# Kernel tuning notes

Measured on AMD Instinct MI355X. Metric: run time of the kernel, lower is better.

## Reference

```python
import jax, jax.numpy as jnp
import numpy as np
import math

DIM = 128
B, S = 4, 4096


def setup_inputs() -> dict:
    key = jax.random.key(0)
    k1, k2, k3, k4 = jax.random.split(key, 4)
    inp = jax.random.normal(k1, (B, S, DIM), dtype=jnp.float32)
    w_k = jax.random.normal(k2, (DIM, DIM), dtype=jnp.float32) / math.sqrt(DIM)
    w_v = jax.random.normal(k3, (DIM, DIM), dtype=jnp.float32) / math.sqrt(DIM)
    mask = jax.random.randint(k4, (B, S, S), 0, 2).astype(jnp.bool_)
    return {"inp": inp, "w_k": w_k, "w_v": w_v, "mask": mask}


def reference(inp, w_k, w_v, mask):
    # key/val projections: BottleLinear(dim, dim, bias=False) -> x @ W^T
    key = jnp.einsum('bsd,ed->bse', inp, w_k)   # [B,S,D]
    val = jnp.einsum('bsd,ed->bse', inp, w_v)   # [B,S,D]
    # score = inp @ key^T / sqrt(dim)           # [B,S,S]
    score = jnp.einsum('bqd,bkd->bqk', inp, key) / math.sqrt(inp.shape[-1])
    score = jnp.where(mask, -jnp.inf, score)
    attn = jax.nn.softmax(score, axis=2)        # [B,S,S]
    out = jnp.einsum('bqk,bkd->bqd', attn, val) # [B,S,D]
    return (out, attn)
```

## Files before the change

### kernel.cpp

```cpp
#include <hip/hip_runtime.h>
#include <hip/hip_fp16.h>
#include <math.h>

#define DIM 128
#define SQL 4096
#define NBATCH 4
#define NROW (NBATCH*SQL)
#define SCALE 0.08838834764831845f
#define KSPLIT 4
#define PROJBLK (NROW/16)
#define MASKBLK 8192

typedef _Float16 f16;
typedef _Float16 f16x4 __attribute__((ext_vector_type(4)));
typedef _Float16 f16x8 __attribute__((ext_vector_type(8)));
typedef float f32x4 __attribute__((ext_vector_type(4)));

__device__ __forceinline__ f32x4 mfma16(f16x8 a, f16x8 b, f32x4 c) {
  return __builtin_amdgcn_mfma_f32_16x16x32_f16(a, b, c, 0, 0, 0);
}

__global__ __launch_bounds__(256) void prep(const float* __restrict__ inp,
                                            const float* __restrict__ wk,
                                            const float* __restrict__ wv,
                                            const void* __restrict__ mask,
                                            f16* __restrict__ q16,
                                            f16* __restrict__ kfrag,
                                            f16* __restrict__ vfrag,
                                            unsigned long long* __restrict__ mbits,
                                            int n) {
  __shared__ float s_in[16][DIM];
  __shared__ __align__(16) f16 s_vt[DIM][16];
  __shared__ __align__(16) f16 s_kf[2048];
  __shared__ int s_is32;
  const int t = threadIdx.x;

  if (blockIdx.x < PROJBLK) {
    const int rowbase = blockIdx.x * 16;
    const int e = t & 127;
    const int half_ = t >> 7;

    for (int r = half_; r < 16; r += 2)
      s_in[r][e] = inp[(size_t)(rowbase + r) * DIM + e];
    __syncthreads();

    float ak[8], av[8];
#pragma unroll
    for (int i = 0; i < 8; ++i) { ak[i] = 0.f; av[i] = 0.f; }

    for (int d0 = 0; d0 < DIM; d0 += 8) {
      float wkl[8], wvl[8];
#pragma unroll
      for (int j = 0; j < 8; ++j) {
        wkl[j] = wk[(size_t)e * DIM + d0 + j];
        wvl[j] = wv[(size_t)e * DIM + d0 + j];
      }
#pragma unroll
      for (int i = 0; i < 8; ++i) {
        const int r = half_ * 8 + i;
#pragma unroll
        for (int j = 0; j < 8; ++j) {
          const float x = s_in[r][d0 + j];
          ak[i] += x * wkl[j];
          av[i] += x * wvl[j];
        }
      }
    }

    const int koff = (e >> 5) * 512 + ((e >> 3) & 3) * 128 + (e & 7);
#pragma unroll
    for (int i = 0; i < 8; ++i) {
      const int r = half_ * 8 + i;
      s_kf[koff + r * 8] = (f16)ak[i];
      q16[(size_t)(rowbase + r) * DIM + e] = (f16)s_in[r][e];
      s_vt[e][r] = (f16)av[i];
    }
    __syncthreads();

    *(f16x8*)(kfrag + ((size_t)(rowbase >> 4)) * 2048 + t * 8) =
        *(const f16x8*)&s_kf[t * 8];

    const int b    = rowbase / SQL;
    const int srow = rowbase % SQL;
    const int m    = (srow >> 4) & 3;
    const int kc2_ = m >> 1, qh = m & 1;
    const int dt_ = t >> 5, h8 = (t >> 4) & 1, l15_ = t & 15;
    const f16x8 vv = *(const f16x8*)&s_vt[dt_ * 16 + l15_][h8 * 8];
    *(f16x8*)(vfrag + ((size_t)b * 64 + (srow >> 6)) * 8192 +
              dt_ * 1024 + kc2_ * 512 + (2 * qh + h8) * 128 + l15_ * 8) = vv;
    return;
  }

  if (t == 0) {
    const unsigned int* w = (const unsigned int*)mask;
    int ok = 1;
    for (int i = 0; i < 64; ++i) ok &= (w[i] <= 1u);
    s_is32 = ok;
  }
  __syncthreads();
  const int mb_bid = blockIdx.x - PROJBLK;
  const int stride = MASKBLK * 256;
  const uint4* mv = (const uint4*)mask;

  if (s_is32) {
    const int nvec = n >> 2;
    for (int i = mb_bid * 256 + t; i < nvec; i += stride) {
      const uint4 v = mv[i];
      const unsigned int nib = (v.x != 0u) | ((v.y != 0u) << 1) |
                               ((v.z != 0u) << 2) | ((v.w != 0u) << 3);
      unsigned long long bits = (unsigned long long)nib << ((i & 15) * 4);
      bits |= __shfl_xor(bits, 1);
      bits |= __shfl_xor(bits, 2);
      bits |= __shfl_xor(bits, 4);
      bits |= __shfl_xor(bits, 8);
      if ((t & 15) == 0) mbits[i >> 4] = bits;
    }
  } else {
    const int nvec = n >> 4;
    for (int i = mb_bid * 256 + t; i < nvec; i += stride) {
      const uint4 v = mv[i];
      const unsigned int M = 0x01020408u;
      unsigned int x;
      x = ((v.x | ((v.x & 0x7F7F7F7Fu) + 0x7F7F7F7Fu)) >> 7) & 0x01010101u;
      const unsigned int n0 = ((x * M) >> 24) & 0xFu;
      x = ((v.y | ((v.y & 0x7F7F7F7Fu) + 0x7F7F7F7Fu)) >> 7) & 0x01010101u;
      const unsigned int n1 = ((x * M) >> 24) & 0xFu;
      x = ((v.z | ((v.z & 0x7F7F7F7Fu) + 0x7F7F7F7Fu)) >> 7) & 0x01010101u;
      const unsigned int n2 = ((x * M) >> 24) & 0xFu;
      x = ((v.w | ((v.w & 0x7F7F7F7Fu) + 0x7F7F7F7Fu)) >> 7) & 0x01010101u;
      const unsigned int n3 = ((x * M) >> 24) & 0xFu;
      const unsigned int b16 = n0 | (n1 << 4) | (n2 << 8) | (n3 << 12);
      unsigned long long bits = (unsigned long long)b16 << ((i & 3) * 16);
      bits |= __shfl_xor(bits, 1);
      bits |= __shfl_xor(bits, 2);
      if ((t & 3) == 0) mbits[i >> 2] = bits;
    }
  }
}

template<int SPILLF16>
__global__ __launch_bounds__(256) void fused(const f16* __restrict__ q16,
                                             const f16* __restrict__ kfrag,
                                             const f16* __restrict__ vfrag,
                                             const unsigned long long* __restrict__ mbits,
                                             float* __restrict__ lpart,
                                             float* __restrict__ opart,
                                             f16* __restrict__ p16,
                                             float* __restrict__ attn) {
  __shared__ __align__(16) f16 pbuf[4][16][72];
  const int kc      = blockIdx.x & (KSPLIT - 1);
  const int blkrow  = (blockIdx.x >> 2) * 64;
  const int b = blkrow / SQL;
  const int lane = threadIdx.x & 63;
  const int w = threadIdx.x >> 6;
  const int rowbase = blkrow + w * 16;
  const int l15 = lane & 15, quad = lane >> 4;

  f16x8 qa[4];
  {
    const f16* qp = q16 + (size_t)(rowbase + l15) * DIM + quad * 8;
#pragma unroll
    for (int c = 0; c < 4; ++c) qa[c] = *(const f16x8*)(qp + c * 32);
  }

  float l[4];
#pragma unroll
  for (int r = 0; r < 4; ++r) l[r] = 0.f;

  f32x4 oacc[8];
#pragma unroll
  for (int dt = 0; dt < 8; ++dt) oacc[dt] = (f32x4){0.f, 0.f, 0.f, 0.f};

  const f16* vf0 = vfrag + (size_t)b * 64 * 8192 + lane * 8;

  const int kb0 = kc * (SQL / KSPLIT);
  for (int kb = kb0; kb < kb0 + SQL / KSPLIT; kb += 64) {
    const size_t rt0 = (size_t)((b * SQL + kb) >> 4);
    f32x4 acc[4];
#pragma unroll
    for (int kt = 0; kt < 4; ++kt) {
      f32x4 a = {0.f, 0.f, 0.f, 0.f};
      const f16* kp = kfrag + (rt0 + kt) * 2048 + lane * 8;
#pragma unroll
      for (int c = 0; c < 4; ++c)
        a = mfma16(qa[c], *(const f16x8*)(kp + c * 512), a);
      acc[kt] = a;
    }
#pragma unroll
    for (int reg = 0; reg < 4; ++reg) {
      const int row = quad * 4 + reg;
      const int rg = rowbase + row;
      const unsigned long long mb = mbits[(size_t)rg * (SQL / 64) + (kb >> 6)];
#pragma unroll
      for (int kt = 0; kt < 4; ++kt) {
        float sv = acc[kt][reg] * SCALE;
        if ((mb >> (kt * 16 + l15)) & 1ull) sv = -1e30f;
        const float e = __expf(sv);
        l[reg] += e;
        pbuf[w][row][kt * 16 + l15] = (f16)e;
      }
    }
    if (SPILLF16) {
#pragma unroll
      for (int s = 0; s < 2; ++s) {
        const int r  = s * 8 + (lane >> 3);
        const int c0 = (lane & 7) * 8;
        const f16x8 v = *(const f16x8*)&pbuf[w][r][c0];
        __builtin_nontemporal_store(v, (f16x8*)(p16 + (size_t)(rowbase + r) * SQL + kb + c0));
      }
    } else {
#pragma unroll
      for (int s = 0; s < 4; ++s) {
        const int r  = s * 4 + (lane >> 4);
        const int c0 = (lane & 15) * 4;
        const f16x4 v = *(const f16x4*)&pbuf[w][r][c0];
        f32x4 o;
#pragma unroll
        for (int j = 0; j < 4; ++j) o[j] = (float)v[j];
        __builtin_nontemporal_store(o, (f32x4*)(attn + (size_t)(rowbase + r) * SQL + kb + c0));
      }
    }
    const f16* vft = vf0 + (size_t)(kb >> 6) * 8192;
#pragma unroll
    for (int kc2 = 0; kc2 < 2; ++kc2) {
      const f16x8 pa = *(const f16x8*)(&pbuf[w][l15][kc2 * 32 + quad * 8]);
#pragma unroll
      for (int dt = 0; dt < 8; ++dt)
        oacc[dt] = mfma16(pa, *(const f16x8*)(vft + dt * 1024 + kc2 * 512), oacc[dt]);
    }
  }

#pragma unroll
  for (int reg = 0; reg < 4; ++reg) {
#pragma unroll
    for (int off = 1; off < 16; off <<= 1) l[reg] += __shfl_xor(l[reg], off);
    if (l15 == 0) lpart[(size_t)kc * NROW + rowbase + quad * 4 + reg] = l[reg];
  }
#pragma unroll
  for (int dt = 0; dt < 8; ++dt)
#pragma unroll
    for (int reg = 0; reg < 4; ++reg)
      opart[(size_t)kc * NROW * DIM +
            (size_t)(rowbase + quad * 4 + reg) * DIM + dt * 16 + l15] = oacc[dt][reg];
}

__global__ __launch_bounds__(256) void rowprep(const float* __restrict__ lpart,
                                               const float* __restrict__ opart,
                                               float* __restrict__ ilrow,
                                               float* __restrict__ out) {
  const int r  = blockIdx.x * 8 + (threadIdx.x >> 5);
  const int d4 = (threadIdx.x & 31) * 4;
  float s = 0.f;
#pragma unroll
  for (int kc = 0; kc < KSPLIT; ++kc) s += lpart[(size_t)kc * NROW + r];
  const float il = 1.f / s;
  f32x4 o = {0.f, 0.f, 0.f, 0.f};
#pragma unroll
  for (int kc = 0; kc < KSPLIT; ++kc) {
    const f32x4 v = *(const f32x4*)&opart[((size_t)kc * NROW + r) * DIM + d4];
    o[0] += v[0]; o[1] += v[1]; o[2] += v[2]; o[3] += v[3];
  }
  o[0] *= il; o[1] *= il; o[2] *= il; o[3] *= il;
  *(f32x4*)&out[(size_t)r * DIM + d4] = o;
  if ((threadIdx.x & 31) == 0) ilrow[r] = il;
}

template<int SPILLF16>
__global__ __launch_bounds__(256) void attnscale(const f16* __restrict__ p16,
                                                 const float* __restrict__ ilrow,
                                                 float* __restrict__ attn) {
  const long long stride = (long long)gridDim.x * blockDim.x;
  if (SPILLF16) {
    const long long nchunk = (long long)NROW * SQL / 8;
    const f16x8* src = (const f16x8*)p16;
    f32x4* dst = (f32x4*)attn;
    for (long long c = (long long)blockIdx.x * blockDim.x + threadIdx.x;
         c < nchunk; c += stride) {
      const float il = ilrow[c >> 9];
      const f16x8 v = __builtin_nontemporal_load(src + c);
      f32x4 a, b2;
      a[0] = (float)v[0] * il; a[1] = (float)v[1] * il;
      a[2] = (float)v[2] * il; a[3] = (float)v[3] * il;
      b2[0] = (float)v[4] * il; b2[1] = (float)v[5] * il;
      b2[2] = (float)v[6] * il; b2[3] = (float)v[7] * il;
      __builtin_nontemporal_store(a, dst + 2 * c);
      __builtin_nontemporal_store(b2, dst + 2 * c + 1);
    }
  } else {
    const long long nchunk = (long long)NROW * SQL / 4;
    f32x4* dst = (f32x4*)attn;
    for (long long c = (long long)blockIdx.x * blockDim.x + threadIdx.x;
         c < nchunk; c += stride) {
      const float il = ilrow[c >> 10];
      f32x4 v = dst[c];
      v[0] *= il; v[1] *= il; v[2] *= il; v[3] *= il;
      __builtin_nontemporal_store(v, dst + c);
    }
  }
}

extern "C" void kernel_launch(void* const* d_in, const int* in_sizes, int n_in,
                              void* d_out, int out_size, void* d_ws, size_t ws_size,
                              hipStream_t stream) {
  const float* inp  = (const float*)d_in[0];
  const float* wk   = (const float*)d_in[1];
  const float* wv   = (const float*)d_in[2];
  const void*  mask = d_in[3];

  float* out  = (float*)d_out;
  float* attn = out + (size_t)NROW * DIM;

  char* ws = (char*)d_ws;
  f16* q16   = (f16*)ws;
  f16* kfrag = q16 + (size_t)NROW * DIM;
  f16* vfrag = kfrag + (size_t)NROW * DIM;
  unsigned long long* mbits =
      (unsigned long long*)(vfrag + (size_t)NROW * DIM);
  char* p = (char*)mbits + (size_t)NROW * (SQL / 8);
  float* lpart = (float*)p; p += (size_t)KSPLIT * NROW * sizeof(float);
  float* ilrow = (float*)p; p += (size_t)NROW * sizeof(float);
  float* opart = (float*)p; p += (size_t)KSPLIT * NROW * DIM * sizeof(float);
  f16*   p16   = (f16*)p;
  const size_t need = (size_t)(p - ws) + (size_t)NROW * SQL * sizeof(f16);
  const bool spill = ws_size >= need;

  prep<<<PROJBLK + MASKBLK, 256, 0, stream>>>(inp, wk, wv, mask,
                                              q16, kfrag, vfrag, mbits,
                                              NBATCH * SQL * SQL);
  if (spill) {
    fused<1><<<(NROW / 64) * KSPLIT, 256, 0, stream>>>(q16, kfrag, vfrag, mbits,
                                                       lpart, opart, p16, attn);
    rowprep<<<NROW / 8, 256, 0, stream>>>(lpart, opart, ilrow, out);
    attnscale<1><<<4096, 256, 0, stream>>>(p16, ilrow, attn);
  } else {
    fused<0><<<(NROW / 64) * KSPLIT, 256, 0, stream>>>(q16, kfrag, vfrag, mbits,
                                                       lpart, opart, p16, attn);
    rowprep<<<NROW / 8, 256, 0, stream>>>(lpart, opart, ilrow, out);
    attnscale<0><<<4096, 256, 0, stream>>>(p16, ilrow, attn);
  }
}
```

Baseline: 718.9 us.

## Interleave mask packing with projection, double KSPLIT, double-buffer P tiles

The prep kernel no longer uses separate projection and mask blocks. Every block now does both, with odd and even blocks ordering the mask packing and the projection differently so memory-bound and compute-bound phases overlap. The fused kernel raises KSPLIT from 4 to 8 and alternates between two LDS P buffers across an unrolled pair of 64-key tiles, giving more blocks and more latency hiding. Nontemporal stores and loads on the f16 spill buffer become ordinary accesses, presumably so the spill can stay in cache. The cost is twice as many opart partials to write and reduce, and more LDS per block.

```diff
diff --git a/kernel.cpp b/kernel.cpp
--- a/kernel.cpp
+++ b/kernel.cpp
@@ -7,9 +7,8 @@
 #define NBATCH 4
 #define NROW (NBATCH*SQL)
 #define SCALE 0.08838834764831845f
-#define KSPLIT 4
-#define PROJBLK (NROW/16)
-#define MASKBLK 8192
+#define KSPLIT 8
+#define PREPBLK (NROW/16)
 
 typedef _Float16 f16;
 typedef _Float16 f16x4 __attribute__((ext_vector_type(4)));
@@ -34,20 +33,64 @@
   __shared__ __align__(16) f16 s_kf[2048];
   __shared__ int s_is32;
   const int t = threadIdx.x;
-
-  if (blockIdx.x < PROJBLK) {
-    const int rowbase = blockIdx.x * 16;
-    const int e = t & 127;
-    const int half_ = t >> 7;
-
-    for (int r = half_; r < 16; r += 2)
-      s_in[r][e] = inp[(size_t)(rowbase + r) * DIM + e];
-    __syncthreads();
-
+  const int bid = blockIdx.x;
+  const int rowbase = bid * 16;
+  const int e = t & 127;
+  const int half_ = t >> 7;
+
+  if (t == 0) {
+    const unsigned int* w = (const unsigned int*)mask;
+    int ok = 1;
+    for (int i = 0; i < 64; ++i) ok &= (w[i] <= 1u);
+    s_is32 = ok;
+  }
+  for (int r = half_; r < 16; r += 2)
+    s_in[r][e] = inp[(size_t)(rowbase + r) * DIM + e];
+  __syncthreads();
+
+  auto maskwork = [&]() {
+    const int stride = PREPBLK * 256;
+    const uint4* mv = (const uint4*)mask;
+    if (s_is32) {
+      const int nvec = n >> 2;
+      for (int i = bid * 256 + t; i < nvec; i += stride) {
+        const uint4 v = mv[i];
+        const unsigned int nib = (v.x != 0u) | ((v.y != 0u) << 1) |
+                                 ((v.z != 0u) << 2) | ((v.w != 0u) << 3);
+        unsigned long long bits = (unsigned long long)nib << ((i & 15) * 4);
+        bits |= __shfl_xor(bits, 1);
+        bits |= __shfl_xor(bits, 2);
+        bits |= __shfl_xor(bits, 4);
+        bits |= __shfl_xor(bits, 8);
+        if ((t & 15) == 0) mbits[i >> 4] = bits;
+      }
+    } else {
+      const int nvec = n >> 4;
+      for (int i = bid * 256 + t; i < nvec; i += stride) {
+        const uint4 v = mv[i];
+        const unsigned int M = 0x01020408u;
+        unsigned int x;
+        x = ((v.x | ((v.x & 0x7F7F7F7Fu) + 0x7F7F7F7Fu)) >> 7) & 0x01010101u;
+        const unsigned int n0 = ((x * M) >> 24) & 0xFu;
+        x = ((v.y | ((v.y & 0x7F7F7F7Fu) + 0x7F7F7F7Fu)) >> 7) & 0x01010101u;
+        const unsigned int n1 = ((x * M) >> 24) & 0xFu;
+        x = ((v.z | ((v.z & 0x7F7F7F7Fu) + 0x7F7F7F7Fu)) >> 7) & 0x01010101u;
+        const unsigned int n2 = ((x * M) >> 24) & 0xFu;
+        x = ((v.w | ((v.w & 0x7F7F7F7Fu) + 0x7F7F7F7Fu)) >> 7) & 0x01010101u;
+        const unsigned int n3 = ((x * M) >> 24) & 0xFu;
+        const unsigned int b16 = n0 | (n1 << 4) | (n2 << 8) | (n3 << 12);
+        unsigned long long bits = (unsigned long long)b16 << ((i & 3) * 16);
+        bits |= __shfl_xor(bits, 1);
+        bits |= __shfl_xor(bits, 2);
+        if ((t & 3) == 0) mbits[i >> 2] = bits;
+      }
+    }
+  };
+
+  auto projcompute = [&]() {
     float ak[8], av[8];
 #pragma unroll
     for (int i = 0; i < 8; ++i) { ak[i] = 0.f; av[i] = 0.f; }
-
     for (int d0 = 0; d0 < DIM; d0 += 8) {
       float wkl[8], wvl[8];
 #pragma unroll
@@ -66,7 +109,6 @@
         }
       }
     }
-
     const int koff = (e >> 5) * 512 + ((e >> 3) & 3) * 128 + (e & 7);
 #pragma unroll
     for (int i = 0; i < 8; ++i) {
@@ -75,11 +117,11 @@
       q16[(size_t)(rowbase + r) * DIM + e] = (f16)s_in[r][e];
       s_vt[e][r] = (f16)av[i];
     }
-    __syncthreads();
-
+  };
+
+  auto projcopyout = [&]() {
     *(f16x8*)(kfrag + ((size_t)(rowbase >> 4)) * 2048 + t * 8) =
         *(const f16x8*)&s_kf[t * 8];
-
     const int b    = rowbase / SQL;
     const int srow = rowbase % SQL;
     const int m    = (srow >> 4) & 3;
@@ -88,53 +130,18 @@
     const f16x8 vv = *(const f16x8*)&s_vt[dt_ * 16 + l15_][h8 * 8];
     *(f16x8*)(vfrag + ((size_t)b * 64 + (srow >> 6)) * 8192 +
               dt_ * 1024 + kc2_ * 512 + (2 * qh + h8) * 128 + l15_ * 8) = vv;
-    return;
-  }
-
-  if (t == 0) {
-    const unsigned int* w = (const unsigned int*)mask;
-    int ok = 1;
-    for (int i = 0; i < 64; ++i) ok &= (w[i] <= 1u);
-    s_is32 = ok;
-  }
-  __syncthreads();
-  const int mb_bid = blockIdx.x - PROJBLK;
-  const int stride = MASKBLK * 256;
-  const uint4* mv = (const uint4*)mask;
-
-  if (s_is32) {
-    const int nvec = n >> 2;
-    for (int i = mb_bid * 256 + t; i < nvec; i += stride) {
-      const uint4 v = mv[i];
-      const unsigned int nib = (v.x != 0u) | ((v.y != 0u) << 1) |
-                               ((v.z != 0u) << 2) | ((v.w != 0u) << 3);
-      unsigned long long bits = (unsigned long long)nib << ((i & 15) * 4);
-      bits |= __shfl_xor(bits, 1);
-      bits |= __shfl_xor(bits, 2);
-      bits |= __shfl_xor(bits, 4);
-      bits |= __shfl_xor(bits, 8);
-      if ((t & 15) == 0) mbits[i >> 4] = bits;
-    }
+  };
+
+  if (bid & 1) {
+    maskwork();
+    projcompute();
+    __syncthreads();
+    projcopyout();
   } else {
-    const int nvec = n >> 4;
-    for (int i = mb_bid * 256 + t; i < nvec; i += stride) {
-      const uint4 v = mv[i];
-      const unsigned int M = 0x01020408u;
-      unsigned int x;
-      x = ((v.x | ((v.x & 0x7F7F7F7Fu) + 0x7F7F7F7Fu)) >> 7) & 0x01010101u;
-      const unsigned int n0 = ((x * M) >> 24) & 0xFu;
-      x = ((v.y | ((v.y & 0x7F7F7F7Fu) + 0x7F7F7F7Fu)) >> 7) & 0x01010101u;
-      const unsigned int n1 = ((x * M) >> 24) & 0xFu;
-      x = ((v.z | ((v.z & 0x7F7F7F7Fu) + 0x7F7F7F7Fu)) >> 7) & 0x01010101u;
-      const unsigned int n2 = ((x * M) >> 24) & 0xFu;
-      x = ((v.w | ((v.w & 0x7F7F7F7Fu) + 0x7F7F7F7Fu)) >> 7) & 0x01010101u;
-      const unsigned int n3 = ((x * M) >> 24) & 0xFu;
-      const unsigned int b16 = n0 | (n1 << 4) | (n2 << 8) | (n3 << 12);
-      unsigned long long bits = (unsigned long long)b16 << ((i & 3) * 16);
-      bits |= __shfl_xor(bits, 1);
-      bits |= __shfl_xor(bits, 2);
-      if ((t & 3) == 0) mbits[i >> 2] = bits;
-    }
+    projcompute();
+    __syncthreads();
+    projcopyout();
+    maskwork();
   }
 }
 
@@ -147,9 +154,9 @@
                                              float* __restrict__ opart,
                                              f16* __restrict__ p16,
                                              float* __restrict__ attn) {
-  __shared__ __align__(16) f16 pbuf[4][16][72];
+  __shared__ __align__(16) f16 pbuf[4][2][16][72];
   const int kc      = blockIdx.x & (KSPLIT - 1);
-  const int blkrow  = (blockIdx.x >> 2) * 64;
+  const int blkrow  = (blockIdx.x >> 3) * 64;
   const int b = blkrow / SQL;
   const int lane = threadIdx.x & 63;
   const int w = threadIdx.x >> 6;
@@ -173,8 +180,7 @@
 
   const f16* vf0 = vfrag + (size_t)b * 64 * 8192 + lane * 8;
 
-  const int kb0 = kc * (SQL / KSPLIT);
-  for (int kb = kb0; kb < kb0 + SQL / KSPLIT; kb += 64) {
+  auto body = [&](int kb, f16 (*pb)[72]) {
     const size_t rt0 = (size_t)((b * SQL + kb) >> 4);
     f32x4 acc[4];
 #pragma unroll
@@ -197,7 +203,7 @@
         if ((mb >> (kt * 16 + l15)) & 1ull) sv = -1e30f;
         const float e = __expf(sv);
         l[reg] += e;
-        pbuf[w][row][kt * 16 + l15] = (f16)e;
+        pb[row][kt * 16 + l15] = (f16)e;
       }
     }
     if (SPILLF16) {
@@ -205,15 +211,15 @@
       for (int s = 0; s < 2; ++s) {
         const int r  = s * 8 + (lane >> 3);
         const int c0 = (lane & 7) * 8;
-        const f16x8 v = *(const f16x8*)&pbuf[w][r][c0];
-        __builtin_nontemporal_store(v, (f16x8*)(p16 + (size_t)(rowbase + r) * SQL + kb + c0));
+        *(f16x8*)(p16 + (size_t)(rowbase + r) * SQL + kb + c0) =
+            *(const f16x8*)&pb[r][c0];
       }
     } else {
 #pragma unroll
       for (int s = 0; s < 4; ++s) {
         const int r  = s * 4 + (lane >> 4);
         const int c0 = (lane & 15) * 4;
-        const f16x4 v = *(const f16x4*)&pbuf[w][r][c0];
+        const f16x4 v = *(const f16x4*)&pb[r][c0];
         f32x4 o;
 #pragma unroll
         for (int j = 0; j < 4; ++j) o[j] = (float)v[j];
@@ -223,11 +229,17 @@
     const f16* vft = vf0 + (size_t)(kb >> 6) * 8192;
 #pragma unroll
     for (int kc2 = 0; kc2 < 2; ++kc2) {
-      const f16x8 pa = *(const f16x8*)(&pbuf[w][l15][kc2 * 32 + quad * 8]);
+      const f16x8 pa = *(const f16x8*)(&pb[l15][kc2 * 32 + quad * 8]);
 #pragma unroll
       for (int dt = 0; dt < 8; ++dt)
         oacc[dt] = mfma16(pa, *(const f16x8*)(vft + dt * 1024 + kc2 * 512), oacc[dt]);
     }
+  };
+
+  const int kb0 = kc * (SQL / KSPLIT);
+  for (int kb = kb0; kb < kb0 + SQL / KSPLIT; kb += 128) {
+    body(kb,      pbuf[w][0]);
+    body(kb + 64, pbuf[w][1]);
   }
 
 #pragma unroll
@@ -277,7 +289,7 @@
     for (long long c = (long long)blockIdx.x * blockDim.x + threadIdx.x;
          c < nchunk; c += stride) {
       const float il = ilrow[c >> 9];
-      const f16x8 v = __builtin_nontemporal_load(src + c);
+      const f16x8 v = src[c];
       f32x4 a, b2;
       a[0] = (float)v[0] * il; a[1] = (float)v[1] * il;
       a[2] = (float)v[2] * il; a[3] = (float)v[3] * il;
@@ -324,9 +336,8 @@
   const size_t need = (size_t)(p - ws) + (size_t)NROW * SQL * sizeof(f16);
   const bool spill = ws_size >= need;
 
-  prep<<<PROJBLK + MASKBLK, 256, 0, stream>>>(inp, wk, wv, mask,
-                                              q16, kfrag, vfrag, mbits,
-                                              NBATCH * SQL * SQL);
+  prep<<<PREPBLK, 256, 0, stream>>>(inp, wk, wv, mask, q16, kfrag, vfrag,
+                                    mbits, NBATCH * SQL * SQL);
   if (spill) {
     fused<1><<<(NROW / 64) * KSPLIT, 256, 0, stream>>>(q16, kfrag, vfrag, mbits,
                                                        lpart, opart, p16, attn);
```

New measurement: 812.8 us. 13.1% more time.
